# Kernel optimization log

Measured on AMD Instinct MI355X. Metric: run time of the kernel, lower is better.

The kernel has to match this reference:

```python
import jax, jax.numpy as jnp
import numpy as np

B, T, C, H, W = 8, 10, 1, 64, 64
HID = 64

def conv2d_same(x, w):
    return jax.lax.conv_general_dilated(x, w, (1, 1), 'SAME', dimension_numbers=('NCHW', 'OIHW', 'NCHW'))

def setup_inputs():
    key = jax.random.key(0)
    ks = iter(jax.random.split(key, 32))
    inp = {'x': jax.random.uniform(next(ks), (B, T, C, H, W), jnp.float32)}
    def cell_params(prefix, in_ch):
        # 4 gates (i, f, g, o) stacked along output channels -> fused gate conv
        inp[prefix + '_Wx'] = jax.random.normal(next(ks), (4 * HID, in_ch, 3, 3), jnp.float32) * 0.05
        inp[prefix + '_Wh'] = jax.random.normal(next(ks), (4 * HID, HID, 3, 3), jnp.float32) * 0.05
        inp[prefix + '_Wc'] = jax.random.normal(next(ks), (4, HID, H, W), jnp.float32) * 0.05
        inp[prefix + '_b'] = jax.random.normal(next(ks), (4, HID, H, W), jnp.float32) * 0.05
    cell_params('enc0', C)
    cell_params('enc1', HID)
    cell_params('dec0', HID)
    cell_params('dec1', HID)
    inp['fin_w'] = jax.random.normal(next(ks), (1, HID, 3, 3), jnp.float32) * 0.05
    inp['fin_b'] = jnp.zeros((1,), jnp.float32)
    inp['prediction_len'] = 10
    return inp

def _cell(Wx, Wh, Wc, b, xt, h, c):
    # gate = act(W_x*x + W_h*h + W_c.c + bias); all 4 gates use the OLD (h, c)
    hid = h.shape[1]
    pre = conv2d_same(xt, Wx) + conv2d_same(h, Wh)  # (B, 4*hid, H, W)
    pre = pre.reshape(pre.shape[0], 4, hid, pre.shape[2], pre.shape[3])
    pre = pre + Wc[None] * c[:, None] + b[None]
    i = jax.nn.sigmoid(pre[:, 0])
    f = jax.nn.sigmoid(pre[:, 1])
    g = jnp.tanh(pre[:, 2])
    o = jax.nn.sigmoid(pre[:, 3])
    c_new = f * c + i * g
    h_new = o * jnp.tanh(c_new)
    return h_new, c_new

def reference(x, enc0_Wx, enc0_Wh, enc0_Wc, enc0_b, enc1_Wx, enc1_Wh, enc1_Wc, enc1_b, dec0_Wx, dec0_Wh, dec0_Wc, dec0_b, dec1_Wx, dec1_Wh, dec1_Wc, dec1_b, fin_w, fin_b, prediction_len):
    b_, t_ = x.shape[0], x.shape[1]
    h_, w_ = x.shape[3], x.shape[4]
    hid = enc0_Wc.shape[1]
    z = jnp.zeros((b_, hid, h_, w_), x.dtype)

    def enc_step(carry, xt):
        h0, c0, h1, c1 = carry
        h0, c0 = _cell(enc0_Wx, enc0_Wh, enc0_Wc, enc0_b, xt, h0, c0)
        h1, c1 = _cell(enc1_Wx, enc1_Wh, enc1_Wc, enc1_b, h0, h1, c1)
        return (h0, c0, h1, c1), None

    (eh0, ec0, eh1, ec1), _ = jax.lax.scan(enc_step, (z, z, z, z), jnp.swapaxes(x, 0, 1))
    state = eh1  # top-layer encoder hidden; decoder h/c start at zeros (as in torch code)

    def dec_step(carry, _):
        s, h0, c0, h1, c1 = carry
        h0, c0 = _cell(dec0_Wx, dec0_Wh, dec0_Wc, dec0_b, s, h0, c0)
        h1, c1 = _cell(dec1_Wx, dec1_Wh, dec1_Wc, dec1_b, h0, h1, c1)
        return (h1, h0, c0, h1, c1), h1

    _, ys = jax.lax.scan(dec_step, (state, z, z, z, z), None, length=prediction_len)
    # ys: (F, B, hid, H, W); Conv3d with (1,3,3) kernel == per-frame 2d conv
    f_ = ys.shape[0]
    y = ys.reshape(f_ * b_, hid, h_, w_)
    y = conv2d_same(y, fin_w) + fin_b[None, :, None, None]
    y = y.reshape(f_, b_, 1, h_, w_)
    return jax.nn.sigmoid(jnp.swapaxes(y, 0, 1))  # (B, F, 1, H, W)
```

## Files before the change

kernel.cpp:

```cpp
#include <hip/hip_runtime.h>
#include <hip/hip_bf16.h>
#include <math.h>

#define BSZ    8
#define TSTEPS 10
#define FLEN   10
#define HID    64
#define HW     4096
#define IMG    (HID * HW)
#define OC4    (4 * HID)
#define PADW   66
#define PPIX   (PADW * PADW)
#define PADIMG (PPIX * HID)
#define PADSZ  (BSZ * PADIMG)
#define SB     (BSZ * IMG)
#define KT_E0  640
#define KT_STD 1152

typedef __attribute__((ext_vector_type(8))) short bf16x8;
typedef __attribute__((ext_vector_type(4))) float f32x4;

__device__ __forceinline__ float sigmoidf_(float x) {
    return 1.0f / (1.0f + __expf(-x));
}
__device__ __forceinline__ float tanh_fast(float x) {
    float e = __expf(2.0f * x);
    return 1.0f - 2.0f / (e + 1.0f);
}
__device__ __forceinline__ float bf2f(short u) {
    union { unsigned u; float f; } cv;
    cv.u = ((unsigned)(unsigned short)u) << 16;
    return cv.f;
}
__device__ __forceinline__ short f2bf(float x) {
    __hip_bfloat16 h = __float2bfloat16(x);
    union { __hip_bfloat16 h; short s; } cv; cv.h = h;
    return cv.s;
}

__global__ __launch_bounds__(256) void reorder_w(
    const float* __restrict__ Wx, int icx,
    const float* __restrict__ Wh, __hip_bfloat16* __restrict__ Bw, int ktot) {
    int ocp = blockIdx.x, hid = ocp >> 2, gate = ocp & 3;
    int oc = gate * 64 + hid;
    for (int k = threadIdx.x; k < ktot; k += 256) {
        int c = k >> 6, j = k & 63;
        float v;
        if (icx == 1) {
            if (c == 0) v = (j < 9) ? Wx[oc * 9 + j] : 0.0f;
            else        v = Wh[(oc * 64 + j) * 9 + (c - 1)];
        } else {
            if (c < 9)  v = Wx[(oc * 64 + j) * 9 + c];
            else        v = Wh[(oc * 64 + j) * 9 + (c - 9)];
        }
        Bw[ocp * ktot + k] = __float2bfloat16(v);
    }
}

__global__ __launch_bounds__(256) void pack_wcb(
    const float* __restrict__ Wc, const float* __restrict__ bias,
    __hip_bfloat16* __restrict__ wcb) {
    int i = blockIdx.x * 256 + threadIdx.x;
    int hid = i >> 12, p = i & 4095;
    union { short s[8]; bf16x8 v; } u;
#pragma unroll
    for (int g = 0; g < 4; g++) {
        u.s[g]     = f2bf(Wc[(g * HID + hid) * HW + p]);
        u.s[4 + g] = f2bf(bias[(g * HID + hid) * HW + p]);
    }
    *(bf16x8*)&wcb[(size_t)i * 8] = u.v;
}

__global__ __launch_bounds__(256) void pack_x_all(
    const float* __restrict__ x, __hip_bfloat16* __restrict__ px_all) {
    int i = blockIdx.x * 256 + threadIdx.x;
    if (i >= TSTEPS * BSZ * PPIX) return;
    int t = i / (BSZ * PPIX);
    int rem = i - t * (BSZ * PPIX);
    int b = rem / PPIX;
    int pp = rem - b * PPIX;
    int y = pp / PADW, xx = pp - y * PADW;
    int oy = y - 1, ox = xx - 1;
    const float* xb = x + ((size_t)(b * TSTEPS + t)) * HW;
    bool interior = (oy >= 0 && oy < 64 && ox >= 0 && ox < 64);
    union { short s[16]; bf16x8 v[2]; } u;
#pragma unroll
    for (int tap = 0; tap < 9; tap++) {
        int yy = oy + tap / 3 - 1, xc = ox + tap % 3 - 1;
        float val = (interior && yy >= 0 && yy < 64 && xc >= 0 && xc < 64)
                        ? xb[yy * 64 + xc] : 0.0f;
        u.s[tap] = f2bf(val);
    }
#pragma unroll
    for (int tap = 9; tap < 16; tap++) u.s[tap] = 0;
    short* o = (short*)(px_all + (size_t)t * PADSZ + ((size_t)(b * PPIX + pp)) * HID);
    *(bf16x8*)&o[0] = u.v[0];
    *(bf16x8*)&o[8] = u.v[1];
}

struct CellArgs {
    const __hip_bfloat16* Bw;
    const __hip_bfloat16* src0;
    const __hip_bfloat16* src1;
    const __hip_bfloat16* wcb;
    float* cbuf;
    __hip_bfloat16* hout;
    int ktot;
    int n0;
    int first;
};

__global__ __launch_bounds__(256) void gemm_cell_fused(CellArgs A0, CellArgs A1) {
    __shared__ short As[128 * 64];
    __shared__ short Bs[128 * 64];
    const bool z1 = (blockIdx.z != 0);
    const __hip_bfloat16* __restrict__ Bw   = z1 ? A1.Bw   : A0.Bw;
    const __hip_bfloat16* __restrict__ src0 = z1 ? A1.src0 : A0.src0;
    const __hip_bfloat16* __restrict__ src1 = z1 ? A1.src1 : A0.src1;
    const __hip_bfloat16* __restrict__ wcb  = z1 ? A1.wcb  : A0.wcb;
    float* __restrict__ cbuf                = z1 ? A1.cbuf : A0.cbuf;
    __hip_bfloat16* __restrict__ hout       = z1 ? A1.hout : A0.hout;
    const int ktot  = z1 ? A1.ktot  : A0.ktot;
    const int n0    = z1 ? A1.n0    : A0.n0;
    const int first = z1 ? A1.first : A0.first;

    const int tid  = threadIdx.x;
    const int lane = tid & 63;
    const int wave = tid >> 6;
    const int quad = lane >> 4;
    const int l15  = lane & 15;
    const int wr = wave >> 1;
    const int wc = wave & 1;
    const int px0 = blockIdx.x * 128;
    const int oc0 = blockIdx.y * 128;

    int a_off[4], s_off[4];
#pragma unroll
    for (int it = 0; it < 4; it++) {
        int idx = it * 256 + tid;
        int rr = idx >> 3, seg = idx & 7;
        int segx = seg ^ (rr & 7);
        a_off[it] = (oc0 + rr) * ktot + segx * 8;
        int px = px0 + rr;
        int b = px >> 12, p = px & 4095, y = p >> 6, x = p & 63;
        s_off[it] = ((b * PADW + y + 1) * PADW + (x + 1)) * HID + segx * 8;
    }
    const int ldsbase = (tid & ~63) * 8;
    const int xa = l15 & 7;

    f32x4 acc[4][4] = {};
    const int nchunks = n0 + 9;

    for (int kk = 0; kk < nchunks; kk++) {
        const __hip_bfloat16* src;
        int tap;
        if (kk < n0) { src = src0; tap = (n0 == 1) ? 4 : kk; }
        else         { src = src1; tap = kk - n0; }
        int dd = ((tap / 3) - 1) * (PADW * HID) + ((tap % 3) - 1) * HID;
        int ka = kk * 64;
#pragma unroll
        for (int it = 0; it < 4; it++) {
            __builtin_amdgcn_global_load_lds(
                (const __attribute__((address_space(1))) void*)(Bw + a_off[it] + ka),
                (__attribute__((address_space(3))) void*)(&As[it * 2048 + ldsbase]),
                16, 0, 0);
            __builtin_amdgcn_global_load_lds(
                (const __attribute__((address_space(1))) void*)(src + s_off[it] + dd),
                (__attribute__((address_space(3))) void*)(&Bs[it * 2048 + ldsbase]),
                16, 0, 0);
        }
        __syncthreads();
#pragma unroll
        for (int k2 = 0; k2 < 2; k2++) {
            int sA = ((k2 * 4 + quad) ^ xa) * 8;
            bf16x8 af[4], bfr[4];
#pragma unroll
            for (int i = 0; i < 4; i++)
                af[i] = *(const bf16x8*)&As[(wr * 64 + i * 16 + l15) * 64 + sA];
#pragma unroll
            for (int j = 0; j < 4; j++)
                bfr[j] = *(const bf16x8*)&Bs[(wc * 64 + j * 16 + l15) * 64 + sA];
#pragma unroll
            for (int i = 0; i < 4; i++)
#pragma unroll
                for (int j = 0; j < 4; j++)
                    acc[i][j] = __builtin_amdgcn_mfma_f32_16x16x32_bf16(
                        af[i], bfr[j], acc[i][j], 0, 0, 0);
        }
        __syncthreads();
    }

    short* hl = As;
    const int hid0 = oc0 >> 2;
#pragma unroll
    for (int i = 0; i < 4; i++) {
        int hidl = wr * 16 + i * 4 + quad;
        int hid = hid0 + hidl;
#pragma unroll
        for (int j = 0; j < 4; j++) {
            int pxl = wc * 64 + j * 16 + l15;
            int px = px0 + pxl;
            int b = px >> 12, p = px & 4095;
            size_t ci = ((size_t)(b * HID + hid)) * HW + p;
            float cv = first ? 0.0f : cbuf[ci];
            bf16x8 wv = *(const bf16x8*)&wcb[((size_t)hid * HW + p) * 8];
            float pg[4];
#pragma unroll
            for (int r = 0; r < 4; r++)
                pg[r] = acc[i][j][r] + bf2f(wv[r]) * cv + bf2f(wv[4 + r]);
            float ig = sigmoidf_(pg[0]);
            float fg = sigmoidf_(pg[1]);
            float gg = tanh_fast(pg[2]);
            float og = sigmoidf_(pg[3]);
            float cn = fg * cv + ig * gg;
            cbuf[ci] = cn;
            float hn = og * tanh_fast(cn);
            hl[pxl * 40 + hidl] = f2bf(hn);
        }
    }
    __syncthreads();
#pragma unroll
    for (int rnd = 0; rnd < 2; rnd++) {
        int task = rnd * 256 + tid;
        int pxl = task >> 2, q = task & 3;
        bf16x8 v = *(const bf16x8*)&hl[pxl * 40 + q * 8];
        int px = px0 + pxl;
        int b = px >> 12, p = px & 4095, y = p >> 6, x = p & 63;
        *(bf16x8*)&hout[((size_t)((b * PADW + y + 1) * PADW + (x + 1))) * HID
                        + hid0 + q * 8] = v;
    }
}

__global__ __launch_bounds__(256) void final_conv(
    const __hip_bfloat16* __restrict__ ph, const float* __restrict__ fw,
    const float* __restrict__ fb, float* __restrict__ out, int f) {
    int b = blockIdx.y;
    int p = blockIdx.x * 256 + threadIdx.x;
    int y = p >> 6, x = p & 63;
    float acc = fb[0];
#pragma unroll
    for (int tap = 0; tap < 9; tap++) {
        const bf16x8* base = (const bf16x8*)(
            ph + ((b * PADW + y + (tap / 3)) * PADW + (x + (tap % 3))) * HID);
#pragma unroll
        for (int c8 = 0; c8 < 8; c8++) {
            bf16x8 v = base[c8];
#pragma unroll
            for (int jj = 0; jj < 8; jj++)
                acc = fmaf(bf2f(v[jj]), fw[(c8 * 8 + jj) * 9 + tap], acc);
        }
    }
    out[((size_t)(b * FLEN + f)) * HW + p] = sigmoidf_(acc);
}

extern "C" void kernel_launch(void* const* d_in, const int* in_sizes, int n_in,
                              void* d_out, int out_size, void* d_ws, size_t ws_size,
                              hipStream_t stream) {
    const float* x = (const float*)d_in[0];
    const float* Wx_[4] = {(const float*)d_in[1], (const float*)d_in[5],
                           (const float*)d_in[9], (const float*)d_in[13]};
    const float* Wh_[4] = {(const float*)d_in[2], (const float*)d_in[6],
                           (const float*)d_in[10], (const float*)d_in[14]};
    const float* Wc_[4] = {(const float*)d_in[3], (const float*)d_in[7],
                           (const float*)d_in[11], (const float*)d_in[15]};
    const float* b_[4]  = {(const float*)d_in[4], (const float*)d_in[8],
                           (const float*)d_in[12], (const float*)d_in[16]};
    const float* fin_w  = (const float*)d_in[17];
    const float* fin_b  = (const float*)d_in[18];
    float* out = (float*)d_out;

    char* wsb = (char*)d_ws;
    const size_t H_BYTES  = 8ull * PADSZ * sizeof(short);
    const size_t PX_BYTES = 10ull * PADSZ * sizeof(short);
    const size_t C_BYTES  = 4ull * SB * sizeof(float);
    const size_t WCB_ELEM = (size_t)HID * HW * 8;

    __hip_bfloat16* hb = (__hip_bfloat16*)wsb;
    __hip_bfloat16* px_all = (__hip_bfloat16*)(wsb + H_BYTES);
    float* cbuf = (float*)(wsb + H_BYTES + PX_BYTES);
    __hip_bfloat16* wcb = (__hip_bfloat16*)(wsb + H_BYTES + PX_BYTES + C_BYTES);
    __hip_bfloat16* bw = wcb + 4 * WCB_ELEM;

    __hip_bfloat16* e0buf[2] = {hb + 0 * (size_t)PADSZ, hb + 1 * (size_t)PADSZ};
    __hip_bfloat16* e1buf[2] = {hb + 2 * (size_t)PADSZ, hb + 3 * (size_t)PADSZ};
    __hip_bfloat16* d0buf[2] = {hb + 4 * (size_t)PADSZ, hb + 5 * (size_t)PADSZ};
    __hip_bfloat16* d1buf[2] = {hb + 6 * (size_t)PADSZ, hb + 7 * (size_t)PADSZ};

    float* ec0 = cbuf + 0 * (size_t)SB;
    float* ec1 = cbuf + 1 * (size_t)SB;
    float* dc0 = cbuf + 2 * (size_t)SB;
    float* dc1 = cbuf + 3 * (size_t)SB;

    __hip_bfloat16* wcb_[4] = {wcb, wcb + WCB_ELEM, wcb + 2 * WCB_ELEM, wcb + 3 * WCB_ELEM};
    __hip_bfloat16* bw_e0 = bw;
    __hip_bfloat16* bw_e1 = bw_e0 + (size_t)OC4 * KT_E0;
    __hip_bfloat16* bw_d0 = bw_e1 + (size_t)OC4 * KT_STD;
    __hip_bfloat16* bw_d1 = bw_d0 + (size_t)OC4 * KT_STD;
    __hip_bfloat16* bw_[4] = {bw_e0, bw_e1, bw_d0, bw_d1};
    float* c_[4] = {ec0, ec1, dc0, dc1};

    hipMemsetAsync(wsb, 0, H_BYTES, stream);

    reorder_w<<<dim3(OC4), 256, 0, stream>>>(Wx_[0], 1,   Wh_[0], bw_e0, KT_E0);
    reorder_w<<<dim3(OC4), 256, 0, stream>>>(Wx_[1], HID, Wh_[1], bw_e1, KT_STD);
    reorder_w<<<dim3(OC4), 256, 0, stream>>>(Wx_[2], HID, Wh_[2], bw_d0, KT_STD);
    reorder_w<<<dim3(OC4), 256, 0, stream>>>(Wx_[3], HID, Wh_[3], bw_d1, KT_STD);
    for (int cix = 0; cix < 4; cix++)
        pack_wcb<<<dim3((HID * HW) / 256), 256, 0, stream>>>(Wc_[cix], b_[cix], wcb_[cix]);
    pack_x_all<<<dim3((TSTEPS * BSZ * PPIX + 255) / 256), 256, 0, stream>>>(x, px_all);

    auto cellargs = [&](int cell, const __hip_bfloat16* s0, const __hip_bfloat16* s1,
                        __hip_bfloat16* ho, int kt, int nn0, int fi) {
        CellArgs a;
        a.Bw = bw_[cell]; a.src0 = s0; a.src1 = s1; a.wcb = wcb_[cell];
        a.cbuf = c_[cell]; a.hout = ho; a.ktot = kt; a.n0 = nn0; a.first = fi;
        return a;
    };
    auto px = [&](int t) { return px_all + (size_t)t * PADSZ; };

    dim3 gfin(16, BSZ);

    {
        CellArgs a = cellargs(0, px(0), e0buf[1], e0buf[0], KT_E0, 1, 1);
        gemm_cell_fused<<<dim3(256, 2, 1), 256, 0, stream>>>(a, a);
    }
    for (int k = 1; k <= 9; k++) {
        int t0 = k, t1 = k - 1;
        CellArgs a0 = cellargs(0, px(t0), e0buf[(t0 - 1) & 1], e0buf[t0 & 1],
                               KT_E0, 1, 0);
        CellArgs a1 = cellargs(1, e0buf[t1 & 1], e1buf[(t1 - 1) & 1], e1buf[t1 & 1],
                               KT_STD, 9, (t1 == 0) ? 1 : 0);
        gemm_cell_fused<<<dim3(256, 2, 2), 256, 0, stream>>>(a0, a1);
    }
    {
        CellArgs a = cellargs(1, e0buf[1], e1buf[0], e1buf[1], KT_STD, 9, 0);
        gemm_cell_fused<<<dim3(256, 2, 1), 256, 0, stream>>>(a, a);
    }
    __hip_bfloat16* enc_top = e1buf[1];

    for (int f = 0; f < FLEN; f++) {
        const __hip_bfloat16* s = (f == 0) ? enc_top : d1buf[(f - 1) & 1];
        CellArgs a0 = cellargs(2, s, d0buf[(f - 1) & 1], d0buf[f & 1],
                               KT_STD, 9, (f == 0) ? 1 : 0);
        gemm_cell_fused<<<dim3(256, 2, 1), 256, 0, stream>>>(a0, a0);
        CellArgs a1 = cellargs(3, d0buf[f & 1], d1buf[(f - 1) & 1], d1buf[f & 1],
                               KT_STD, 9, (f == 0) ? 1 : 0);
        gemm_cell_fused<<<dim3(256, 2, 1), 256, 0, stream>>>(a1, a1);
        final_conv<<<gfin, 256, 0, stream>>>(d1buf[f & 1], fin_w, fin_b, out, f);
    }
}
```

Before: 1.570 ms.

## Double-buffer LDS tiles in gate GEMM and fuse final conv into decoder launch

Loads for the next K-chunk into a second LDS buffer are issued while the current chunk's MFMAs run, with priority raised around the MFMA block. The per-frame final convolution is folded into the following dec0 launch as extra z-slice blocks, removing separate launches. This doubles LDS use per block, which may lower occupancy, and adds mostly idle blocks to the fused launch.

```diff
diff --git a/kernel.cpp b/kernel.cpp
--- a/kernel.cpp
+++ b/kernel.cpp
@@ -110,9 +110,43 @@
     int first;
 };
 
-__global__ __launch_bounds__(256) void gemm_cell_fused(CellArgs A0, CellArgs A1) {
-    __shared__ short As[128 * 64];
-    __shared__ short Bs[128 * 64];
+struct FinArgs {
+    const __hip_bfloat16* ph;
+    const float* fw;
+    const float* fb;
+    float* out;
+    int f;
+    int active;
+};
+
+__global__ __launch_bounds__(256) void gemm_cell_fused(CellArgs A0, CellArgs A1,
+                                                       FinArgs F) {
+    __shared__ short As[2][128 * 64];
+    __shared__ short Bs[2][128 * 64];
+
+    if (blockIdx.z == 1 && F.active) {
+        int id = blockIdx.y * 256 + blockIdx.x;
+        if (id >= 128) return;
+        int b = id >> 4;
+        int p = (id & 15) * 256 + threadIdx.x;
+        int y = p >> 6, x = p & 63;
+        float acc = F.fb[0];
+#pragma unroll
+        for (int tap = 0; tap < 9; tap++) {
+            const bf16x8* base = (const bf16x8*)(
+                F.ph + ((b * PADW + y + (tap / 3)) * PADW + (x + (tap % 3))) * HID);
+#pragma unroll
+            for (int c8 = 0; c8 < 8; c8++) {
+                bf16x8 v = base[c8];
+#pragma unroll
+                for (int jj = 0; jj < 8; jj++)
+                    acc = fmaf(bf2f(v[jj]), F.fw[(c8 * 8 + jj) * 9 + tap], acc);
+            }
+        }
+        F.out[((size_t)(b * FLEN + F.f)) * HW + p] = sigmoidf_(acc);
+        return;
+    }
+
     const bool z1 = (blockIdx.z != 0);
     const __hip_bfloat16* __restrict__ Bw   = z1 ? A1.Bw   : A0.Bw;
     const __hip_bfloat16* __restrict__ src0 = z1 ? A1.src0 : A0.src0;
@@ -151,7 +185,7 @@
     f32x4 acc[4][4] = {};
     const int nchunks = n0 + 9;
 
-    for (int kk = 0; kk < nchunks; kk++) {
+    auto stage = [&](int kk, int buf) {
         const __hip_bfloat16* src;
         int tap;
         if (kk < n0) { src = src0; tap = (n0 == 1) ? 4 : kk; }
@@ -162,35 +196,46 @@
         for (int it = 0; it < 4; it++) {
             __builtin_amdgcn_global_load_lds(
                 (const __attribute__((address_space(1))) void*)(Bw + a_off[it] + ka),
-                (__attribute__((address_space(3))) void*)(&As[it * 2048 + ldsbase]),
+                (__attribute__((address_space(3))) void*)(&As[buf][it * 2048 + ldsbase]),
                 16, 0, 0);
             __builtin_amdgcn_global_load_lds(
                 (const __attribute__((address_space(1))) void*)(src + s_off[it] + dd),
-                (__attribute__((address_space(3))) void*)(&Bs[it * 2048 + ldsbase]),
+                (__attribute__((address_space(3))) void*)(&Bs[buf][it * 2048 + ldsbase]),
                 16, 0, 0);
         }
-        __syncthreads();
+    };
+
+    stage(0, 0);
+    asm volatile("s_waitcnt vmcnt(0)" ::: "memory");
+    __syncthreads();
+
+    for (int kk = 0; kk < nchunks; kk++) {
+        const int cur = kk & 1;
+        if (kk + 1 < nchunks) stage(kk + 1, cur ^ 1);
 #pragma unroll
         for (int k2 = 0; k2 < 2; k2++) {
             int sA = ((k2 * 4 + quad) ^ xa) * 8;
             bf16x8 af[4], bfr[4];
 #pragma unroll
             for (int i = 0; i < 4; i++)
-                af[i] = *(const bf16x8*)&As[(wr * 64 + i * 16 + l15) * 64 + sA];
+                af[i] = *(const bf16x8*)&As[cur][(wr * 64 + i * 16 + l15) * 64 + sA];
 #pragma unroll
             for (int j = 0; j < 4; j++)
-                bfr[j] = *(const bf16x8*)&Bs[(wc * 64 + j * 16 + l15) * 64 + sA];
+                bfr[j] = *(const bf16x8*)&Bs[cur][(wc * 64 + j * 16 + l15) * 64 + sA];
+            __builtin_amdgcn_s_setprio(1);
 #pragma unroll
             for (int i = 0; i < 4; i++)
 #pragma unroll
                 for (int j = 0; j < 4; j++)
                     acc[i][j] = __builtin_amdgcn_mfma_f32_16x16x32_bf16(
                         af[i], bfr[j], acc[i][j], 0, 0, 0);
-        }
+            __builtin_amdgcn_s_setprio(0);
+        }
+        asm volatile("s_waitcnt vmcnt(0)" ::: "memory");
         __syncthreads();
     }
 
-    short* hl = As;
+    short* hl = &As[0][0];
     const int hid0 = oc0 >> 2;
 #pragma unroll
     for (int i = 0; i < 4; i++) {
@@ -318,11 +363,20 @@
     };
     auto px = [&](int t) { return px_all + (size_t)t * PADSZ; };
 
+    FinArgs finoff;
+    finoff.ph = nullptr; finoff.fw = nullptr; finoff.fb = nullptr;
+    finoff.out = nullptr; finoff.f = 0; finoff.active = 0;
+    auto finargs = [&](const __hip_bfloat16* ph, int f) {
+        FinArgs F;
+        F.ph = ph; F.fw = fin_w; F.fb = fin_b; F.out = out; F.f = f; F.active = 1;
+        return F;
+    };
+
     dim3 gfin(16, BSZ);
 
     {
         CellArgs a = cellargs(0, px(0), e0buf[1], e0buf[0], KT_E0, 1, 1);
-        gemm_cell_fused<<<dim3(256, 2, 1), 256, 0, stream>>>(a, a);
+        gemm_cell_fused<<<dim3(256, 2, 1), 256, 0, stream>>>(a, a, finoff);
     }
     for (int k = 1; k <= 9; k++) {
         int t0 = k, t1 = k - 1;
@@ -330,11 +384,11 @@
                                KT_E0, 1, 0);
         CellArgs a1 = cellargs(1, e0buf[t1 & 1], e1buf[(t1 - 1) & 1], e1buf[t1 & 1],
                                KT_STD, 9, (t1 == 0) ? 1 : 0);
-        gemm_cell_fused<<<dim3(256, 2, 2), 256, 0, stream>>>(a0, a1);
+        gemm_cell_fused<<<dim3(256, 2, 2), 256, 0, stream>>>(a0, a1, finoff);
     }
     {
         CellArgs a = cellargs(1, e0buf[1], e1buf[0], e1buf[1], KT_STD, 9, 0);
-        gemm_cell_fused<<<dim3(256, 2, 1), 256, 0, stream>>>(a, a);
+        gemm_cell_fused<<<dim3(256, 2, 1), 256, 0, stream>>>(a, a, finoff);
     }
     __hip_bfloat16* enc_top = e1buf[1];
 
@@ -342,10 +396,14 @@
         const __hip_bfloat16* s = (f == 0) ? enc_top : d1buf[(f - 1) & 1];
         CellArgs a0 = cellargs(2, s, d0buf[(f - 1) & 1], d0buf[f & 1],
                                KT_STD, 9, (f == 0) ? 1 : 0);
-        gemm_cell_fused<<<dim3(256, 2, 1), 256, 0, stream>>>(a0, a0);
+        if (f == 0)
+            gemm_cell_fused<<<dim3(256, 2, 1), 256, 0, stream>>>(a0, a0, finoff);
+        else
+            gemm_cell_fused<<<dim3(256, 2, 2), 256, 0, stream>>>(
+                a0, a0, finargs(d1buf[(f - 1) & 1], f - 1));
         CellArgs a1 = cellargs(3, d0buf[f & 1], d1buf[(f - 1) & 1], d1buf[f & 1],
                                KT_STD, 9, (f == 0) ? 1 : 0);
-        gemm_cell_fused<<<dim3(256, 2, 1), 256, 0, stream>>>(a1, a1);
-        final_conv<<<gfin, 256, 0, stream>>>(d1buf[f & 1], fin_w, fin_b, out, f);
-    }
-}
+        gemm_cell_fused<<<dim3(256, 2, 1), 256, 0, stream>>>(a1, a1, finoff);
+    }
+    final_conv<<<gfin, 256, 0, stream>>>(d1buf[1], fin_w, fin_b, out, 9);
+}
```

Measured after the change: 2.363 ms. 50.5% more time.
